# Kernel tuning notes

Hardware: AMD Instinct MI355X
Metric: run time of the kernel (lower is better)

The kernel has to match this reference:

```python
import jax, jax.numpy as jnp
import numpy as np

N, E, H, C, G = 10000, 20000, 12, 768, 64  # nodes, edges, heads, per-head dim, graphs
NEG_SLOPE = 0.2


def _gat_layer(x, W, a_src, a_dst, b, src, dst):
    # x: [N, 768], W: [768, H*C], a_src/a_dst: [H, C], b: [C]
    h = (x @ W).reshape(-1, H, C)                      # [N, H, C]
    s = jnp.einsum('nhc,hc->nh', h, a_src)             # alpha_src per node
    d = jnp.einsum('nhc,hc->nh', h, a_dst)             # alpha_dst per node
    e = jax.nn.leaky_relu(s[src] + d[dst], NEG_SLOPE)  # [Etot, H]
    # segment softmax over incoming edges of each destination node
    m = jax.lax.stop_gradient(jax.ops.segment_max(e, dst, num_segments=N))
    ex = jnp.exp(e - m[dst])
    den = jax.ops.segment_sum(ex, dst, num_segments=N)
    alpha = ex / (den[dst] + 1e-16)                    # [Etot, H]
    out = jax.ops.segment_sum(h[src] * alpha[:, :, None], dst, num_segments=N)
    return out.mean(axis=1) + b                        # concat=False -> head mean, [N, C]


def setup_inputs() -> dict:
    key = jax.random.key(0)
    ks = jax.random.split(key, 16)
    sc = 0.02
    f32 = jnp.float32
    return {
        'x': jax.random.normal(ks[0], (N, 768), f32),
        'edge_index': jax.random.randint(ks[1], (2, E), 0, N),
        'batch': jnp.sort(jax.random.randint(ks[2], (N,), 0, G)),
        'W1': (jax.random.normal(ks[3], (768, H * C), f32) * sc),
        'a_src1': (jax.random.normal(ks[4], (H, C), f32) * sc),
        'a_dst1': (jax.random.normal(ks[5], (H, C), f32) * sc),
        'b1': jnp.zeros((C,), f32),
        'W2': (jax.random.normal(ks[6], (768, H * C), f32) * sc),
        'a_src2': (jax.random.normal(ks[7], (H, C), f32) * sc),
        'a_dst2': (jax.random.normal(ks[8], (H, C), f32) * sc),
        'b2': jnp.zeros((C,), f32),
        'mlp_w1': (jax.random.normal(ks[9], (768, 128), f32) * sc),
        'mlp_b1': jnp.zeros((128,), f32),
        'mlp_w2': (jax.random.normal(ks[10], (128, 4), f32) * sc),
        'mlp_b2': jnp.zeros((4,), f32),
    }


def reference(x, edge_index, batch, W1, a_src1, a_dst1, b1, W2, a_src2, a_dst2, b2,
              mlp_w1, mlp_b1, mlp_w2, mlp_b2):
    loops = jnp.arange(N)                               # GATConv add_self_loops=True
    src = jnp.concatenate([edge_index[0], loops])
    dst = jnp.concatenate([edge_index[1], loops])
    h = _gat_layer(x, W1, a_src1, a_dst1, b1, src, dst)
    h = _gat_layer(h, W2, a_src2, a_dst2, b2, src, dst)
    # scatter_mean over graph assignment
    ssum = jax.ops.segment_sum(h, batch, num_segments=G)
    cnt = jax.ops.segment_sum(jnp.ones((N,), h.dtype), batch, num_segments=G)
    g = ssum / jnp.maximum(cnt, 1.0)[:, None]           # [G, 768]
    z = jax.nn.relu(g @ mlp_w1 + mlp_b1)
    return z @ mlp_w2 + mlp_b2                          # [G, 4] logits
```

## Files before the change

kernel.cpp:

```cpp
#include <hip/hip_runtime.h>
#include <stdint.h>

typedef unsigned short u16;
typedef unsigned int   u32;

#define NNODES 10000
#define NEDGES 20000
#define ETOT   30000
#define NHEADS 12
#define CDIM   768
#define FDIM   768
#define KDIM   9216
#define NGRAPH 64
#define MPAD   10112
#define NEG_SLOPE 0.2f
#define DMAX   32

typedef __attribute__((ext_vector_type(8))) short short8;
typedef __attribute__((ext_vector_type(4))) float f32x4;

__device__ __forceinline__ u16 f32_bf16(float f) {
  u32 u = __float_as_uint(f);
  u = (u + 0x7FFFu + ((u >> 16) & 1u)) >> 16;
  return (u16)u;
}
__device__ __forceinline__ float bf16_f32(u16 v) {
  return __uint_as_float(((u32)v) << 16);
}

__global__ void k_count(const int* __restrict__ dste, int* __restrict__ counts) {
  int e = blockIdx.x * blockDim.x + threadIdx.x;
  if (e >= ETOT) return;
  int dst;
  if (e < NEDGES) dst = dste[e]; else dst = e - NEDGES;
  atomicAdd(&counts[dst], 1);
}

__global__ void k_scan(const int* __restrict__ counts, int* __restrict__ offs) {
  __shared__ int part[256];
  int t = threadIdx.x;
  const int chunk = 40;
  int beg = t * chunk;
  int end = beg + chunk; if (end > NNODES) end = NNODES;
  int s = 0;
  for (int i = beg; i < end && i < NNODES; i++) s += counts[i];
  part[t] = s;
  __syncthreads();
  for (int d = 1; d < 256; d <<= 1) {
    int v = (t >= d) ? part[t - d] : 0;
    __syncthreads();
    part[t] += v;
    __syncthreads();
  }
  int base = (t == 0) ? 0 : part[t - 1];
  for (int i = beg; i < end && i < NNODES; i++) { offs[i] = base; base += counts[i]; }
  if (t == 255) offs[NNODES] = base;
}

__global__ void k_seed(const int* __restrict__ offs, int* __restrict__ cursor) {
  int n = blockIdx.x * blockDim.x + threadIdx.x;
  if (n < NNODES) cursor[n] = offs[n];
}

__global__ void k_scatter(const int* __restrict__ dste, int* __restrict__ cursor,
                          int* __restrict__ elist) {
  int e = blockIdx.x * blockDim.x + threadIdx.x;
  if (e >= ETOT) return;
  int dst;
  if (e < NEDGES) dst = dste[e]; else dst = e - NEDGES;
  int pos = atomicAdd(&cursor[dst], 1);
  elist[pos] = e;
}

__global__ void k_U(const float* __restrict__ W, const float* __restrict__ a_src,
                    const float* __restrict__ a_dst, float* __restrict__ Ut) {
  int k = blockIdx.x;
  int t = threadIdx.x, w = t >> 6, l = t & 63;
  const float* Wrow = W + (size_t)k * KDIM;
#pragma unroll
  for (int q = 0; q < 6; q++) {
    int o = w * 6 + q;
    int h = (o < 12) ? o : o - 12;
    const float* av = (o < 12) ? (a_src + h * CDIM) : (a_dst + h * CDIM);
    const float* wr = Wrow + h * CDIM;
    float p = 0.f;
    for (int c = l; c < CDIM; c += 64) p += wr[c] * av[c];
#pragma unroll
    for (int d = 32; d > 0; d >>= 1) p += __shfl_down(p, d, 64);
    if (l == 0) Ut[o * FDIM + k] = p;
  }
}

__global__ void k_sd(const float* __restrict__ xin, const float* __restrict__ Ut,
                     float* __restrict__ sd, u16* __restrict__ xbf) {
  __shared__ float UtS[24 * FDIM];
  int t = threadIdx.x, w = t >> 6, l = t & 63;
  const float4* U4 = (const float4*)Ut;
  float4* S4 = (float4*)UtS;
  for (int i = t; i < 24 * FDIM / 4; i += 256) S4[i] = U4[i];
  __syncthreads();
#pragma unroll
  for (int rep = 0; rep < 5; rep++) {
    int n = blockIdx.x * 20 + w * 5 + rep;
    if (n >= NNODES) continue;
    const float* xr = xin + (size_t)n * FDIM;
    float4 x0 = *(const float4*)(xr + 4 * l);
    float4 x1 = *(const float4*)(xr + 4 * l + 256);
    float4 x2 = *(const float4*)(xr + 4 * l + 512);
    u16* xb = xbf + (size_t)n * FDIM + 4 * l;
    ushort4 p0, p1, p2;
    p0.x = f32_bf16(x0.x); p0.y = f32_bf16(x0.y); p0.z = f32_bf16(x0.z); p0.w = f32_bf16(x0.w);
    p1.x = f32_bf16(x1.x); p1.y = f32_bf16(x1.y); p1.z = f32_bf16(x1.z); p1.w = f32_bf16(x1.w);
    p2.x = f32_bf16(x2.x); p2.y = f32_bf16(x2.y); p2.z = f32_bf16(x2.z); p2.w = f32_bf16(x2.w);
    *(ushort4*)xb = p0;
    *(ushort4*)(xb + 256) = p1;
    *(ushort4*)(xb + 512) = p2;
#pragma unroll
    for (int o = 0; o < 24; o++) {
      const float4* up = (const float4*)(UtS + o * FDIM + 4 * l);
      float4 u0 = up[0];
      float4 u1 = up[64];
      float4 u2 = up[128];
      float a = x0.x * u0.x + x0.y * u0.y + x0.z * u0.z + x0.w * u0.w
              + x1.x * u1.x + x1.y * u1.y + x1.z * u1.z + x1.w * u1.w
              + x2.x * u2.x + x2.y * u2.y + x2.z * u2.z + x2.w * u2.w;
#pragma unroll
      for (int d = 32; d > 0; d >>= 1) a += __shfl_xor(a, d, 64);
      if (l == 0) sd[n * 24 + o] = a;
    }
  }
}

__global__ void k_trans(const float* __restrict__ W, u16* __restrict__ Bt) {
  int kt = blockIdx.x * 32, jt = blockIdx.y * 32;
  int tx = threadIdx.x, ty = threadIdx.y;
  __shared__ float tile[32][33];
#pragma unroll
  for (int r = 0; r < 4; r++)
    tile[ty + 8 * r][tx] = W[(size_t)(kt + ty + 8 * r) * KDIM + jt + tx];
  __syncthreads();
#pragma unroll
  for (int r = 0; r < 4; r++)
    Bt[(size_t)(jt + ty + 8 * r) * FDIM + kt + tx] = f32_bf16(tile[tx][ty + 8 * r]);
}

__global__ __launch_bounds__(256, 2) void k_gemm(const u16* __restrict__ A,
    const u16* __restrict__ B, u16* __restrict__ C) {
  __shared__ __align__(16) u16 As[2][128 * 32];
  __shared__ __align__(16) u16 Bs[2][256 * 32];
  int t = threadIdx.x;
  int w = t >> 6, l = t & 63;
  int col0 = blockIdx.x * 256;
  int row0 = blockIdx.y * 128;
  int wm = (w >> 1) * 64;
  int wn = (w & 1) * 128;
  f32x4 acc[4][8] = {};
  int idx0 = t * 8;
  int idx1 = idx0 + 2048;
  const u16* Ag0 = A + (size_t)(row0 + (idx0 >> 5)) * FDIM + (idx0 & 31);
  const u16* Ag1 = A + (size_t)(row0 + (idx1 >> 5)) * FDIM + (idx1 & 31);
  const u16* Bg0 = B + (size_t)(col0 + (idx0 >> 5)) * FDIM + (idx0 & 31);
  const u16* Bg1 = B + (size_t)(col0 + ((idx0 + 2048) >> 5)) * FDIM + (idx0 & 31);
  const u16* Bg2 = B + (size_t)(col0 + ((idx0 + 4096) >> 5)) * FDIM + (idx0 & 31);
  const u16* Bg3 = B + (size_t)(col0 + ((idx0 + 6144) >> 5)) * FDIM + (idx0 & 31);
  int lr = l & 15, lk = (l >> 4) * 8;

  short8 ra0, ra1, rb0, rb1, rb2, rb3;
  auto gload = [&](int k0) {
    ra0 = *(const short8*)(Ag0 + k0);
    ra1 = *(const short8*)(Ag1 + k0);
    rb0 = *(const short8*)(Bg0 + k0);
    rb1 = *(const short8*)(Bg1 + k0);
    rb2 = *(const short8*)(Bg2 + k0);
    rb3 = *(const short8*)(Bg3 + k0);
  };
  auto swrite = [&](int buf) {
    *(short8*)(&As[buf][idx0]) = ra0;
    *(short8*)(&As[buf][idx1]) = ra1;
    *(short8*)(&Bs[buf][idx0]) = rb0;
    *(short8*)(&Bs[buf][idx0 + 2048]) = rb1;
    *(short8*)(&Bs[buf][idx0 + 4096]) = rb2;
    *(short8*)(&Bs[buf][idx0 + 6144]) = rb3;
  };

  gload(0);
  swrite(0);
  gload(32);
  __syncthreads();
  const int NIT = FDIM / 32;
  int cur = 0;
  for (int it = 0; it < NIT; it++) {
    short8 af[4], bf[8];
#pragma unroll
    for (int i = 0; i < 4; i++) af[i] = *(const short8*)(&As[cur][(wm + i * 16 + lr) * 32 + lk]);
#pragma unroll
    for (int j = 0; j < 8; j++) bf[j] = *(const short8*)(&Bs[cur][(wn + j * 16 + lr) * 32 + lk]);
#pragma unroll
    for (int i = 0; i < 4; i++)
#pragma unroll
      for (int j = 0; j < 8; j++)
        acc[i][j] = __builtin_amdgcn_mfma_f32_16x16x32_bf16(af[i], bf[j], acc[i][j], 0, 0, 0);
    if (it + 1 < NIT) {
      swrite(cur ^ 1);
      if (it + 2 < NIT) gload((it + 2) * 32);
    }
    __syncthreads();
    cur ^= 1;
  }

  int lg = l >> 4;
#pragma unroll
  for (int i = 0; i < 4; i++)
#pragma unroll
    for (int j = 0; j < 8; j++) {
      int col = col0 + wn + j * 16 + lr;
#pragma unroll
      for (int r = 0; r < 4; r++) {
        int row = row0 + wm + i * 16 + lg * 4 + r;
        C[(size_t)row * KDIM + col] = f32_bf16(acc[i][j][r]);
      }
    }
}

__global__ void k_att(const u16* __restrict__ Hbig, const int* __restrict__ ei,
                      const int* __restrict__ offs, const int* __restrict__ elist,
                      const float* __restrict__ sd, const float* __restrict__ bias,
                      float* __restrict__ out) {
  int t = threadIdx.x, w = t >> 6, l = t & 63;
  int n = blockIdx.x * 4 + w;
  __shared__ int   srcsS[4][DMAX];
  __shared__ float alphS[4][NHEADS * DMAX];
  if (n >= NNODES) return;
  int* srcs = srcsS[w];
  float* alph = alphS[w];
  int beg = offs[n];
  int deg = offs[n + 1] - beg;
  if (deg > DMAX) deg = DMAX;
  if (l < deg) {
    int e = elist[beg + l];
    srcs[l] = (e < NEDGES) ? ei[e] : e - NEDGES;
  }
  __builtin_amdgcn_wave_barrier();
  for (int p = l; p < deg * NHEADS; p += 64) {
    int i = p / NHEADS, h = p - i * NHEADS;
    float v = sd[srcs[i] * 24 + h] + sd[n * 24 + 12 + h];
    v = (v > 0.f) ? v : NEG_SLOPE * v;
    alph[h * DMAX + i] = v;
  }
  __builtin_amdgcn_wave_barrier();
  if (l < NHEADS) {
    float m = -1e30f;
    for (int i = 0; i < deg; i++) m = fmaxf(m, alph[l * DMAX + i]);
    float s = 0.f;
    for (int i = 0; i < deg; i++) {
      float ex = expf(alph[l * DMAX + i] - m);
      alph[l * DMAX + i] = ex;
      s += ex;
    }
    float inv = 1.f / (s + 1e-16f);
    for (int i = 0; i < deg; i++) alph[l * DMAX + i] *= inv;
  }
  __builtin_amdgcn_wave_barrier();
#pragma unroll
  for (int pass = 0; pass < 3; pass++) {
    float4 acc = make_float4(0.f, 0.f, 0.f, 0.f);
    for (int i = 0; i < deg; i++) {
      const u16* hb = Hbig + (size_t)srcs[i] * KDIM + pass * 256 + 4 * l;
#pragma unroll
      for (int h = 0; h < NHEADS; h++) {
        ushort4 hv = *(const ushort4*)(hb + h * CDIM);
        float a = alph[h * DMAX + i];
        acc.x += a * bf16_f32(hv.x);
        acc.y += a * bf16_f32(hv.y);
        acc.z += a * bf16_f32(hv.z);
        acc.w += a * bf16_f32(hv.w);
      }
    }
    int c = pass * 256 + 4 * l;
    const float sc = 1.f / 12.f;
    float4 ov;
    ov.x = acc.x * sc + bias[c + 0];
    ov.y = acc.y * sc + bias[c + 1];
    ov.z = acc.z * sc + bias[c + 2];
    ov.w = acc.w * sc + bias[c + 3];
    *(float4*)(out + (size_t)n * FDIM + c) = ov;
  }
}

__global__ void k_pool(const float* __restrict__ h2, const int* __restrict__ batch,
                       float* __restrict__ g) {
  int gi = blockIdx.x;
  int c = blockIdx.y * 256 + threadIdx.x;
  int lo = 0, hi = NNODES;
  while (lo < hi) { int mid = (lo + hi) >> 1; if (batch[mid] < gi) lo = mid + 1; else hi = mid; }
  int start = lo;
  lo = start; hi = NNODES;
  while (lo < hi) { int mid = (lo + hi) >> 1; if (batch[mid] < gi + 1) lo = mid + 1; else hi = mid; }
  int end = lo;
  int cnt = end - start; if (cnt < 1) cnt = 1;
  float inv = 1.f / (float)cnt;
  float s = 0.f;
  for (int n = start; n < end; n++) s += h2[(size_t)n * FDIM + c];
  g[gi * FDIM + c] = s * inv;
}

__global__ void k_mlp(const float* __restrict__ g, const float* __restrict__ w1,
                      const float* __restrict__ b1, const float* __restrict__ w2,
                      const float* __restrict__ b2, float* __restrict__ out) {
  int gi = blockIdx.x;
  int t = threadIdx.x;
  __shared__ float gs[FDIM];
  __shared__ float zs[128];
  for (int i = t; i < FDIM; i += 128) gs[i] = g[gi * FDIM + i];
  __syncthreads();
  float a = b1[t];
  for (int k = 0; k < FDIM; k++) a += gs[k] * w1[k * 128 + t];
  zs[t] = (a > 0.f) ? a : 0.f;
  __syncthreads();
  if (t < 4) {
    float o = b2[t];
    for (int i = 0; i < 128; i++) o += zs[i] * w2[i * 4 + t];
    out[gi * 4 + t] = o;
  }
}

extern "C" void kernel_launch(void* const* d_in, const int* in_sizes, int n_in,
                              void* d_out, int out_size, void* d_ws, size_t ws_size,
                              hipStream_t stream) {
  const float* x    = (const float*)d_in[0];
  const int*   ei   = (const int*)d_in[1];
  const int*   batch= (const int*)d_in[2];
  const float* W1   = (const float*)d_in[3];
  const float* as1  = (const float*)d_in[4];
  const float* ad1  = (const float*)d_in[5];
  const float* b1   = (const float*)d_in[6];
  const float* W2   = (const float*)d_in[7];
  const float* as2  = (const float*)d_in[8];
  const float* ad2  = (const float*)d_in[9];
  const float* b2   = (const float*)d_in[10];
  const float* mw1  = (const float*)d_in[11];
  const float* mb1  = (const float*)d_in[12];
  const float* mw2  = (const float*)d_in[13];
  const float* mb2  = (const float*)d_in[14];
  float* out = (float*)d_out;
  (void)in_sizes; (void)n_in; (void)out_size; (void)ws_size;

  char* wsb = (char*)d_ws;
  size_t off = 0;
  auto alloc = [&](size_t bytes) -> void* {
    void* p = wsb + off;
    off += (bytes + 255) & ~(size_t)255;
    return p;
  };
  u16*  Hbig   = (u16*)alloc((size_t)MPAD * KDIM * 2);
  u16*  Bt     = (u16*)alloc((size_t)KDIM * FDIM * 2);
  float* h1    = (float*)alloc((size_t)NNODES * FDIM * 4);
  float* h2    = (float*)alloc((size_t)NNODES * FDIM * 4);
  u16*  xbf    = (u16*)h2;
  float* sd    = (float*)alloc((size_t)NNODES * 24 * 4);
  float* Ut    = (float*)alloc((size_t)FDIM * 24 * 4);
  int*  counts = (int*)alloc((size_t)NNODES * 4);
  int*  offs   = (int*)alloc((size_t)(NNODES + 1) * 4);
  int*  cursor = (int*)alloc((size_t)NNODES * 4);
  int*  elist  = (int*)alloc((size_t)ETOT * 4);
  float* gbuf  = (float*)alloc((size_t)NGRAPH * FDIM * 4);

  hipMemsetAsync(counts, 0, NNODES * 4, stream);
  k_count<<<(ETOT + 255) / 256, 256, 0, stream>>>(ei + NEDGES, counts);
  k_scan<<<1, 256, 0, stream>>>(counts, offs);
  k_seed<<<(NNODES + 255) / 256, 256, 0, stream>>>(offs, cursor);
  k_scatter<<<(ETOT + 255) / 256, 256, 0, stream>>>(ei + NEDGES, cursor, elist);

  for (int layer = 0; layer < 2; layer++) {
    const float* xin  = layer ? h1  : x;
    const float* W    = layer ? W2  : W1;
    const float* asrc = layer ? as2 : as1;
    const float* adst = layer ? ad2 : ad1;
    const float* bb   = layer ? b2  : b1;
    float* hout       = layer ? h2  : h1;

    k_U<<<FDIM, 256, 0, stream>>>(W, asrc, adst, Ut);
    k_sd<<<(NNODES + 19) / 20, 256, 0, stream>>>(xin, Ut, sd, xbf);
    k_trans<<<dim3(FDIM / 32, KDIM / 32), dim3(32, 8), 0, stream>>>(W, Bt);
    k_gemm<<<dim3(KDIM / 256, MPAD / 128), 256, 0, stream>>>(xbf, Bt, Hbig);
    k_att<<<(NNODES + 3) / 4, 256, 0, stream>>>(Hbig, ei, offs, elist, sd, bb, hout);
  }

  k_pool<<<dim3(NGRAPH, 3), 256, 0, stream>>>(h2, batch, gbuf);
  k_mlp<<<NGRAPH, 128, 0, stream>>>(gbuf, mw1, mb1, mw2, mb2, out);
}
```

Baseline: 875.3 us.

## Rewrite GEMM with 256x256 tiles, direct global-to-LDS loads and swizzled LDS

```diff
diff --git a/kernel.cpp b/kernel.cpp
--- a/kernel.cpp
+++ b/kernel.cpp
@@ -12,7 +12,7 @@
 #define FDIM   768
 #define KDIM   9216
 #define NGRAPH 64
-#define MPAD   10112
+#define MPAD   10240
 #define NEG_SLOPE 0.2f
 #define DMAX   32
 
@@ -144,80 +144,119 @@
     Bt[(size_t)(jt + ty + 8 * r) * FDIM + kt + tx] = f32_bf16(tile[tx][ty + 8 * r]);
 }
 
-__global__ __launch_bounds__(256, 2) void k_gemm(const u16* __restrict__ A,
+#define GLL16(G, L) __builtin_amdgcn_global_load_lds( \
+  (const __attribute__((address_space(1))) void*)(G), \
+  (__attribute__((address_space(3))) void*)(L), 16, 0, 0)
+
+__global__ __launch_bounds__(512, 2) void k_gemm(const u16* __restrict__ A,
     const u16* __restrict__ B, u16* __restrict__ C) {
-  __shared__ __align__(16) u16 As[2][128 * 32];
-  __shared__ __align__(16) u16 Bs[2][256 * 32];
+  __shared__ __align__(16) u16 As[2][256 * 64];
+  __shared__ __align__(16) u16 Bs[2][256 * 64];
   int t = threadIdx.x;
   int w = t >> 6, l = t & 63;
-  int col0 = blockIdx.x * 256;
-  int row0 = blockIdx.y * 128;
-  int wm = (w >> 1) * 64;
-  int wn = (w & 1) * 128;
-  f32x4 acc[4][8] = {};
-  int idx0 = t * 8;
-  int idx1 = idx0 + 2048;
-  const u16* Ag0 = A + (size_t)(row0 + (idx0 >> 5)) * FDIM + (idx0 & 31);
-  const u16* Ag1 = A + (size_t)(row0 + (idx1 >> 5)) * FDIM + (idx1 & 31);
-  const u16* Bg0 = B + (size_t)(col0 + (idx0 >> 5)) * FDIM + (idx0 & 31);
-  const u16* Bg1 = B + (size_t)(col0 + ((idx0 + 2048) >> 5)) * FDIM + (idx0 & 31);
-  const u16* Bg2 = B + (size_t)(col0 + ((idx0 + 4096) >> 5)) * FDIM + (idx0 & 31);
-  const u16* Bg3 = B + (size_t)(col0 + ((idx0 + 6144) >> 5)) * FDIM + (idx0 & 31);
-  int lr = l & 15, lk = (l >> 4) * 8;
-
-  short8 ra0, ra1, rb0, rb1, rb2, rb3;
-  auto gload = [&](int k0) {
-    ra0 = *(const short8*)(Ag0 + k0);
-    ra1 = *(const short8*)(Ag1 + k0);
-    rb0 = *(const short8*)(Bg0 + k0);
-    rb1 = *(const short8*)(Bg1 + k0);
-    rb2 = *(const short8*)(Bg2 + k0);
-    rb3 = *(const short8*)(Bg3 + k0);
-  };
-  auto swrite = [&](int buf) {
-    *(short8*)(&As[buf][idx0]) = ra0;
-    *(short8*)(&As[buf][idx1]) = ra1;
-    *(short8*)(&Bs[buf][idx0]) = rb0;
-    *(short8*)(&Bs[buf][idx0 + 2048]) = rb1;
-    *(short8*)(&Bs[buf][idx0 + 4096]) = rb2;
-    *(short8*)(&Bs[buf][idx0 + 6144]) = rb3;
-  };
-
-  gload(0);
-  swrite(0);
-  gload(32);
-  __syncthreads();
-  const int NIT = FDIM / 32;
-  int cur = 0;
-  for (int it = 0; it < NIT; it++) {
-    short8 af[4], bf[8];
-#pragma unroll
-    for (int i = 0; i < 4; i++) af[i] = *(const short8*)(&As[cur][(wm + i * 16 + lr) * 32 + lk]);
-#pragma unroll
-    for (int j = 0; j < 8; j++) bf[j] = *(const short8*)(&Bs[cur][(wn + j * 16 + lr) * 32 + lk]);
-#pragma unroll
-    for (int i = 0; i < 4; i++)
-#pragma unroll
-      for (int j = 0; j < 8; j++)
-        acc[i][j] = __builtin_amdgcn_mfma_f32_16x16x32_bf16(af[i], bf[j], acc[i][j], 0, 0, 0);
-    if (it + 1 < NIT) {
-      swrite(cur ^ 1);
-      if (it + 2 < NIT) gload((it + 2) * 32);
+  int swz = (blockIdx.x & 7) * 180 + (blockIdx.x >> 3);
+  int by = swz / 36, bx = swz - by * 36;
+  int row0 = by * 256, col0 = bx * 256;
+  int wr = w >> 2, wc = w & 3;
+  int lr = l & 15;
+  int koff = (l >> 4) * 16;
+  int swzr = (lr & 7) << 4;
+  int rb = t >> 3;
+  int csw = ((t & 7) ^ (rb & 7)) * 8;
+  const u16* baseA = A + (size_t)(row0 + rb) * FDIM + csw;
+  const u16* baseB = B + (size_t)(col0 + rb) * FDIM + csw;
+
+  f32x4 acc[8][4] = {};
+  short8 a[4][2], b0[2][2], b1[2][2];
+
+  auto stA = [&](int buf, int h, int s) {
+    const u16* g = baseA + (size_t)(h * 128) * FDIM + s * 64;
+    u16* lp = (u16*)&As[buf][0] + h * 8192 + (w << 9);
+    GLL16(g, lp);
+    GLL16(g + (size_t)64 * FDIM, lp + 4096);
+  };
+  auto stB = [&](int buf, int h, int s) {
+    const u16* g = baseB + (size_t)(h * 128) * FDIM + s * 64;
+    u16* lp = (u16*)&Bs[buf][0] + h * 8192 + (w << 9);
+    GLL16(g, lp);
+    GLL16(g + (size_t)64 * FDIM, lp + 4096);
+  };
+  auto ldA = [&](int buf, int mo) {
+#pragma unroll
+    for (int m = 0; m < 4; m++)
+#pragma unroll
+      for (int c = 0; c < 2; c++) {
+        int row = wr * 128 + (mo + m) * 16 + lr;
+        int off = row * 128 + ((c * 64 + koff) ^ swzr);
+        a[m][c] = *(const short8*)((const char*)&As[buf][0] + off);
+      }
+  };
+  auto ldB = [&](int buf, short8 (*bb)[2], int no) {
+#pragma unroll
+    for (int n = 0; n < 2; n++)
+#pragma unroll
+      for (int c = 0; c < 2; c++) {
+        int row = wc * 64 + (no + n) * 16 + lr;
+        int off = row * 128 + ((c * 64 + koff) ^ swzr);
+        bb[n][c] = *(const short8*)((const char*)&Bs[buf][0] + off);
+      }
+  };
+  auto mm8 = [&](short8 (*bb)[2], int mo, int no) {
+    __builtin_amdgcn_s_setprio(1);
+#pragma unroll
+    for (int m = 0; m < 4; m++)
+#pragma unroll
+      for (int n = 0; n < 2; n++)
+#pragma unroll
+        for (int c = 0; c < 2; c++)
+          acc[mo + m][no + n] = __builtin_amdgcn_mfma_f32_16x16x32_bf16(
+              a[m][c], bb[n][c], acc[mo + m][no + n], 0, 0, 0);
+    __builtin_amdgcn_s_setprio(0);
+  };
+
+  stA(0, 0, 0); stA(0, 1, 0); stB(0, 0, 0); stB(0, 1, 0);
+  stB(1, 0, 1); stA(1, 0, 1);
+  asm volatile("s_waitcnt vmcnt(4)" ::: "memory");
+  __builtin_amdgcn_s_barrier();
+
+#pragma unroll
+  for (int s = 0; s < 12; s++) {
+    int P = s & 1;
+    ldA(P, 0); ldB(P, b0, 0);
+    if (s + 1 < 12) stB(P ^ 1, 1, s + 1);
+    __builtin_amdgcn_s_barrier();
+    mm8(b0, 0, 0);
+    __builtin_amdgcn_s_barrier();
+    ldB(P, b1, 2);
+    if (s + 1 < 12) stA(P ^ 1, 1, s + 1);
+    __builtin_amdgcn_s_barrier();
+    mm8(b1, 0, 2);
+    __builtin_amdgcn_s_barrier();
+    ldA(P, 4);
+    if (s + 2 < 12) stB(P, 0, s + 2);
+    __builtin_amdgcn_s_barrier();
+    mm8(b1, 4, 2);
+    __builtin_amdgcn_s_barrier();
+    if (s + 2 < 12) stA(P, 0, s + 2);
+    __builtin_amdgcn_s_barrier();
+    mm8(b0, 4, 0);
+    if (s < 11) {
+      if (s <= 9) asm volatile("s_waitcnt vmcnt(4)" ::: "memory");
+      else        asm volatile("s_waitcnt vmcnt(0)" ::: "memory");
     }
-    __syncthreads();
-    cur ^= 1;
+    __builtin_amdgcn_s_barrier();
   }
 
   int lg = l >> 4;
 #pragma unroll
-  for (int i = 0; i < 4; i++)
-#pragma unroll
-    for (int j = 0; j < 8; j++) {
-      int col = col0 + wn + j * 16 + lr;
+  for (int m = 0; m < 8; m++)
+#pragma unroll
+    for (int n = 0; n < 4; n++) {
+      int col = col0 + wc * 64 + n * 16 + lr;
 #pragma unroll
       for (int r = 0; r < 4; r++) {
-        int row = row0 + wm + i * 16 + lg * 4 + r;
-        C[(size_t)row * KDIM + col] = f32_bf16(acc[i][j][r]);
+        int row = row0 + wr * 128 + m * 16 + lg * 4 + r;
+        C[(size_t)row * KDIM + col] = f32_bf16(acc[m][n][r]);
       }
     }
 }
@@ -366,6 +405,7 @@
   float* gbuf  = (float*)alloc((size_t)NGRAPH * FDIM * 4);
 
   hipMemsetAsync(counts, 0, NNODES * 4, stream);
+  hipMemsetAsync(xbf + (size_t)NNODES * FDIM, 0, (size_t)(MPAD - NNODES) * FDIM * 2, stream);
   k_count<<<(ETOT + 255) / 256, 256, 0, stream>>>(ei + NEDGES, counts);
   k_scan<<<1, 256, 0, stream>>>(counts, offs);
   k_seed<<<(NNODES + 255) / 256, 256, 0, stream>>>(offs, cursor);
@@ -382,7 +422,7 @@
     k_U<<<FDIM, 256, 0, stream>>>(W, asrc, adst, Ut);
     k_sd<<<(NNODES + 19) / 20, 256, 0, stream>>>(xin, Ut, sd, xbf);
     k_trans<<<dim3(FDIM / 32, KDIM / 32), dim3(32, 8), 0, stream>>>(W, Bt);
-    k_gemm<<<dim3(KDIM / 256, MPAD / 128), 256, 0, stream>>>(xbf, Bt, Hbig);
+    k_gemm<<<dim3((MPAD / 256) * (KDIM / 256)), 512, 0, stream>>>(xbf, Bt, Hbig);
     k_att<<<(NNODES + 3) / 4, 256, 0, stream>>>(Hbig, ei, offs, elist, sd, bb, hout);
   }
 
```

After: 907.7 us. 1.04x slower.
